# Performance work log

Measured on AMD Instinct MI355X. Metric: run time of the kernel, lower is better.

## Reference

```python
import jax, jax.numpy as jnp
import numpy as np

B, S, D, J, NI = 8192, 20, 300, 512, 1000
VG = 2048 + 5 * 6  # vis_dim + 5*6 = guide feature dim


def setup_inputs() -> dict:
    key = jax.random.key(0)
    ks = jax.random.split(key, 11)
    context = jax.random.normal(ks[0], (B, S, D), jnp.float32)
    embedded = jax.random.normal(ks[1], (B, S, D), jnp.float32)
    input_labels = jax.random.randint(ks[2], (B, S), 0, 10000, dtype=jnp.int64)
    # guarantee at least one valid token per row (avoid divide-by-zero renorm)
    input_labels = input_labels.at[:, 0].set(jnp.maximum(input_labels[:, 0], 1))
    guide_input = jax.random.normal(ks[3], (NI, VG), jnp.float32)
    sent_to_image_ann = jax.random.randint(ks[4], (2 * B,), 0, NI, dtype=jnp.int64)
    # parameters (PyTorch Linear: y = x @ W.T + b)
    W_sent = jax.random.normal(ks[5], (J, D), jnp.float32) * 0.02
    b_sent = jnp.zeros((J,), jnp.float32)
    W_emb = jax.random.normal(ks[6], (J, VG), jnp.float32) * 0.02
    b_emb = jnp.zeros((J,), jnp.float32)
    w_fc = jax.random.normal(ks[7], (J,), jnp.float32) * 0.02
    b_fc = jnp.zeros((), jnp.float32)
    return {"context": context, "embedded": embedded, "input_labels": input_labels,
            "guide_input": guide_input, "sent_to_image_ann": sent_to_image_ann,
            "W_sent": W_sent, "b_sent": b_sent, "W_emb": W_emb, "b_emb": b_emb,
            "w_fc": w_fc, "b_fc": b_fc}


def reference(context, embedded, input_labels, guide_input, sent_to_image_ann,
              W_sent, b_sent, W_emb, b_emb, w_fc, b_fc):
    # prefix-valid mask: loop in original breaks at first zero label
    nonzero = (input_labels != 0).astype(jnp.float32)          # (B,S)
    valid = jnp.cumprod(nonzero, axis=1)                        # (B,S)
    # per-sentence guide feature: guide_input[sent_to_image_ann[2*i]]
    fea = guide_input[sent_to_image_ann[::2]]                   # (B,VG)
    # fc_embed(guidance): guidance rows are fea (valid prefix) or 0 (else),
    # so the linear output is fea@W_emb.T+b_emb or just b_emb.
    fea_emb = fea @ W_emb.T + b_emb                             # (B,J)
    guid_emb = valid[:, :, None] * fea_emb[:, None, :] + (1.0 - valid)[:, :, None] * b_emb
    cxt_emb = jnp.einsum('bsd,jd->bsj', context, W_sent) + b_sent
    H = jnp.tanh(cxt_emb + guid_emb)                            # (B,S,J)
    scores = jnp.einsum('bsj,j->bs', H, w_fc) + b_fc            # (B,S)
    attn = jax.nn.softmax(scores, axis=1)
    attn = attn * nonzero
    attn = attn / jnp.sum(attn, axis=1, keepdims=True)
    weighted_cxt = jnp.einsum('bs,bsd->bd', attn, embedded)     # (B,D)
    return weighted_cxt
```

## Files before the change

### kernel.cpp

```cpp
#include <hip/hip_runtime.h>
#include <hip/hip_bf16.h>

#define BB 8192
#define SS 20
#define DD 300
#define JJ 512
#define NII 1000
#define VGG 2078
#define KP 328
#define RBY 656
#define BTILE 41984
#define BP1 72

typedef __attribute__((ext_vector_type(8))) short short8v;
typedef __attribute__((ext_vector_type(4))) float float4v;

__device__ __forceinline__ float tanh_fast(float x) {
    float t = __expf(2.f * x);
    return 1.f - 2.f * __builtin_amdgcn_rcpf(t + 1.f);
}

__device__ __forceinline__ unsigned short bf16u(float x) {
    __hip_bfloat16 h = __float2bfloat16(x);
    return *(unsigned short*)&h;
}

__device__ __forceinline__ void gload16(const void* g, void* l) {
    __builtin_amdgcn_global_load_lds(
        (const __attribute__((address_space(1))) unsigned int*)g,
        (__attribute__((address_space(3))) unsigned int*)l, 16, 0, 0);
}

__global__ __launch_bounds__(256) void kc_pad_bf16(const float* __restrict__ src,
                                                   __hip_bfloat16* __restrict__ dst,
                                                   int rows, int scols, int dcols) {
    int idx = blockIdx.x * 256 + threadIdx.x;
    if (idx >= rows * dcols) return;
    int r = idx / dcols, c = idx % dcols;
    float v = (c < scols) ? src[(long)r * scols + c] : 0.f;
    dst[idx] = __float2bfloat16(v);
}

__global__ __launch_bounds__(256) void k0_valid(const int* __restrict__ labels,
                                                float* __restrict__ valid,
                                                float* __restrict__ nonzero) {
    int b = blockIdx.x * blockDim.x + threadIdx.x;
    if (b >= BB) return;
    float v = 1.f;
    for (int s = 0; s < SS; ++s) {
        float nz = (labels[b * SS + s] != 0) ? 1.f : 0.f;
        v *= nz;
        nonzero[b * SS + s] = nz;
        valid[b * SS + s] = v;
    }
}

__global__ __launch_bounds__(256) void k1_femb_mfma(
    const __hip_bfloat16* __restrict__ Gb,
    const __hip_bfloat16* __restrict__ Web,
    const float* __restrict__ b_emb,
    __hip_bfloat16* __restrict__ femb) {
    __shared__ __hip_bfloat16 Al[64 * BP1];
    __shared__ __hip_bfloat16 Bl[64 * BP1];
    const int t = threadIdx.x;
    const int m0 = blockIdx.x * 64;
    const int n0 = blockIdx.y * 64;
    const int lane = t & 63;
    const int w = t >> 6;
    const int wm = w >> 1, wn = w & 1;
    const int li = lane & 15, lq = lane >> 4;

    float4v acc[2][2] = {};

    for (int kt = 0; kt < 33; ++kt) {
        for (int c = t; c < 512; c += 256) {
            int rr = c >> 3, off = (c & 7) * 8;
            int gr = m0 + rr; if (gr > NII - 1) gr = NII - 1;
            *(uint4*)&Al[rr * BP1 + off] =
                *(const uint4*)(Gb + (long)gr * 2112 + kt * 64 + off);
            *(uint4*)&Bl[rr * BP1 + off] =
                *(const uint4*)(Web + (long)(n0 + rr) * 2112 + kt * 64 + off);
        }
        __syncthreads();
#pragma unroll
        for (int ks = 0; ks < 2; ++ks) {
            short8v a[2], b[2];
#pragma unroll
            for (int mt = 0; mt < 2; ++mt)
                a[mt] = *(const short8v*)&Al[(wm * 32 + mt * 16 + li) * BP1 + ks * 32 + lq * 8];
#pragma unroll
            for (int nt = 0; nt < 2; ++nt)
                b[nt] = *(const short8v*)&Bl[(wn * 32 + nt * 16 + li) * BP1 + ks * 32 + lq * 8];
#pragma unroll
            for (int mt = 0; mt < 2; ++mt)
#pragma unroll
                for (int nt = 0; nt < 2; ++nt)
                    acc[mt][nt] = __builtin_amdgcn_mfma_f32_16x16x32_bf16(
                        a[mt], b[nt], acc[mt][nt], 0, 0, 0);
        }
        __syncthreads();
    }
#pragma unroll
    for (int nt = 0; nt < 2; ++nt) {
        int col = n0 + wn * 32 + nt * 16 + li;
        float be = b_emb[col];
#pragma unroll
        for (int mt = 0; mt < 2; ++mt)
#pragma unroll
            for (int reg = 0; reg < 4; ++reg) {
                int row = wm * 32 + mt * 16 + lq * 4 + reg;
                femb[(long)(m0 + row) * JJ + col] = __float2bfloat16(acc[mt][nt][reg] + be);
            }
    }
}

__global__ __launch_bounds__(256) void k2_scores_mfma(
    const float* __restrict__ context,
    const __hip_bfloat16* __restrict__ Wsb,
    const float* __restrict__ b_sent,
    const float* __restrict__ w_fc,
    const float* __restrict__ b_fc,
    const __hip_bfloat16* __restrict__ femb,
    const int* __restrict__ ann,
    const float* __restrict__ b_emb,
    const float* __restrict__ valid,
    float* __restrict__ scores) {
    __shared__ __align__(16) char smem[48128];
    char* buf  = smem;
    char* fl   = smem + 41984;
    float* red = (float*)(smem + 47104);

    const int t = threadIdx.x;
    const int m0 = blockIdx.x * 64;
    const int b_lo = m0 / SS;
    const int lane = t & 63;
    const int w = t >> 6;
    const int wm = w >> 1, wn = w & 1;
    const int li = lane & 15, lq = lane >> 4;

    for (int idx = t; idx < 64 * 82; idx += 256) {
        int r = idx / 82, q = idx - r * 82;
        ushort4 pk;
        if (q < 75) {
            float4 v = *(const float4*)(context + (long)(m0 + r) * DD + q * 4);
            pk.x = bf16u(v.x); pk.y = bf16u(v.y); pk.z = bf16u(v.z); pk.w = bf16u(v.w);
        } else { pk.x = pk.y = pk.z = pk.w = 0; }
        *(ushort4*)(buf + r * RBY + q * 8) = pk;
    }
    if (t < 320) {
        int i = t >> 6, ch = t & 63;
        int b = b_lo + i; if (b > BB - 1) b = BB - 1;
        int grow = ann[2 * b];
        *(uint4*)(fl + i * 1024 + ch * 16) =
            *(const uint4*)(femb + (long)grow * JJ + ch * 8);
    }
    int brel0_0 = 0, brel0_1 = 0, selbits = 0, vbits = 0;
#pragma unroll
    for (int mt = 0; mt < 2; ++mt) {
        int base = m0 + wm * 32 + mt * 16 + lq * 4;
        int br0 = base / SS - b_lo;
        if (mt == 0) brel0_0 = br0; else brel0_1 = br0;
#pragma unroll
        for (int reg = 0; reg < 4; ++reg) {
            int m = base + reg;
            int slot = mt * 4 + reg;
            if (m / SS - b_lo != br0) selbits |= (1 << slot);
            if (valid[m] != 0.f)      vbits  |= (1 << slot);
        }
    }
    __syncthreads();

    short8v areg[2][10];
#pragma unroll
    for (int mt = 0; mt < 2; ++mt) {
        int r = wm * 32 + mt * 16 + li;
#pragma unroll
        for (int kt = 0; kt < 10; ++kt)
            areg[mt][kt] = *(const short8v*)(buf + r * RBY + kt * 64 + lq * 16);
    }
    __syncthreads();

    float sp[8] = {0.f, 0.f, 0.f, 0.f, 0.f, 0.f, 0.f, 0.f};
    const int rbB0 = (wn * 32 + li) * RBY;
    const int rbB1 = (wn * 32 + 16 + li) * RBY;

    for (int jt = 0; jt < 8; ++jt) {
        const char* gB = (const char*)Wsb + (long)jt * BTILE;
        const int wbase = w * 656;
#pragma unroll
        for (int i = 0; i < 10; ++i)
            gload16(gB + (long)(wbase + i * 64 + lane) * 16,
                    buf + (wbase + i * 64) * 16);
        if (lane < 16)
            gload16(gB + (long)(wbase + 640 + lane) * 16,
                    buf + (wbase + 640) * 16);
        __syncthreads();

        float4v acc[2][2] = {};
#pragma unroll
        for (int kt = 0; kt < 10; ++kt) {
            short8v b0 = *(const short8v*)(buf + rbB0 + kt * 64 + lq * 16);
            short8v b1 = *(const short8v*)(buf + rbB1 + kt * 64 + lq * 16);
            acc[0][0] = __builtin_amdgcn_mfma_f32_16x16x32_bf16(areg[0][kt], b0, acc[0][0], 0, 0, 0);
            acc[0][1] = __builtin_amdgcn_mfma_f32_16x16x32_bf16(areg[0][kt], b1, acc[0][1], 0, 0, 0);
            acc[1][0] = __builtin_amdgcn_mfma_f32_16x16x32_bf16(areg[1][kt], b0, acc[1][0], 0, 0, 0);
            acc[1][1] = __builtin_amdgcn_mfma_f32_16x16x32_bf16(areg[1][kt], b1, acc[1][1], 0, 0, 0);
        }

#pragma unroll
        for (int nt = 0; nt < 2; ++nt) {
            int col = jt * 64 + wn * 32 + nt * 16 + li;
            float bs = b_sent[col], wf = w_fc[col], be = b_emb[col];
#pragma unroll
            for (int mt = 0; mt < 2; ++mt) {
                int br = (mt == 0) ? brel0_0 : brel0_1;
                int br1 = (br < 4) ? br + 1 : 4;
                float f0 = __bfloat162float(*(const __hip_bfloat16*)(fl + br  * 1024 + col * 2));
                float f1 = __bfloat162float(*(const __hip_bfloat16*)(fl + br1 * 1024 + col * 2));
#pragma unroll
                for (int reg = 0; reg < 4; ++reg) {
                    int slot = mt * 4 + reg;
                    float fv = ((selbits >> slot) & 1) ? f1 : f0;
                    float g  = ((vbits  >> slot) & 1) ? fv : be;
                    sp[slot] += tanh_fast(acc[mt][nt][reg] + bs + g) * wf;
                }
            }
        }
        __syncthreads();
    }

#pragma unroll
    for (int slot = 0; slot < 8; ++slot) {
        float v = sp[slot];
        v += __shfl_xor(v, 1); v += __shfl_xor(v, 2);
        v += __shfl_xor(v, 4); v += __shfl_xor(v, 8);
        sp[slot] = v;
    }
    if (li == 0) {
#pragma unroll
        for (int mt = 0; mt < 2; ++mt)
#pragma unroll
            for (int reg = 0; reg < 4; ++reg)
                red[wn * 64 + wm * 32 + mt * 16 + lq * 4 + reg] = sp[mt * 4 + reg];
    }
    __syncthreads();
    if (t < 64) scores[m0 + t] = red[t] + red[64 + t] + b_fc[0];
}

__global__ __launch_bounds__(256) void k3_out(const float* __restrict__ scores,
                                              const float* __restrict__ nonzero,
                                              const float* __restrict__ embedded,
                                              float* __restrict__ out) {
    __shared__ float wgt[3][SS];
    const int b0 = blockIdx.x * 3;
    const int t = threadIdx.x;
    if (t < 3) {
        int b = b0 + t;
        if (b < BB) {
            float sc[SS], nz[SS];
            float mx = -1e30f;
            for (int s = 0; s < SS; ++s) {
                sc[s] = scores[b * SS + s];
                nz[s] = nonzero[b * SS + s];
                mx = fmaxf(mx, sc[s]);
            }
            float den = 0.f, e[SS];
            for (int s = 0; s < SS; ++s) { e[s] = nz[s] * __expf(sc[s] - mx); den += e[s]; }
            float inv = 1.f / den;
            for (int s = 0; s < SS; ++s) wgt[t][s] = e[s] * inv;
        }
    }
    __syncthreads();
    if (t < 225) {
        int r = t / 75, q = t - r * 75;
        int b = b0 + r;
        if (b < BB) {
            float4 a; a.x = a.y = a.z = a.w = 0.f;
#pragma unroll
            for (int s = 0; s < SS; ++s) {
                float4 e = *(const float4*)(embedded + ((long)b * SS + s) * DD + q * 4);
                float ww = wgt[r][s];
                a.x += ww * e.x; a.y += ww * e.y; a.z += ww * e.z; a.w += ww * e.w;
            }
            *(float4*)(out + (long)b * DD + q * 4) = a;
        }
    }
}

extern "C" void kernel_launch(void* const* d_in, const int* in_sizes, int n_in,
                              void* d_out, int out_size, void* d_ws, size_t ws_size,
                              hipStream_t stream) {
    const float* context  = (const float*)d_in[0];
    const float* embedded = (const float*)d_in[1];
    const int*   labels   = (const int*)d_in[2];
    const float* guide    = (const float*)d_in[3];
    const int*   ann      = (const int*)d_in[4];
    const float* W_sent   = (const float*)d_in[5];
    const float* b_sent   = (const float*)d_in[6];
    const float* W_emb    = (const float*)d_in[7];
    const float* b_emb    = (const float*)d_in[8];
    const float* w_fc     = (const float*)d_in[9];
    const float* b_fc     = (const float*)d_in[10];
    float* out = (float*)d_out;

    char* w = (char*)d_ws;
    __hip_bfloat16* femb = (__hip_bfloat16*)(w);
    float* valid         = (float*)(w + 1048576);
    float* nonzero       = (float*)(w + 1703936);
    float* scores        = (float*)(w + 2359296);
    __hip_bfloat16* Wsb  = (__hip_bfloat16*)(w + 3014656);
    __hip_bfloat16* Web  = (__hip_bfloat16*)(w + 3350528);
    __hip_bfloat16* Gb   = (__hip_bfloat16*)(w + 5513216);

    hipLaunchKernelGGL(kc_pad_bf16, dim3((JJ * KP + 255) / 256), dim3(256), 0, stream,
                       W_sent, Wsb, JJ, DD, KP);
    hipLaunchKernelGGL(kc_pad_bf16, dim3((JJ * 2112 + 255) / 256), dim3(256), 0, stream,
                       W_emb, Web, JJ, VGG, 2112);
    hipLaunchKernelGGL(kc_pad_bf16, dim3((NII * 2112 + 255) / 256), dim3(256), 0, stream,
                       guide, Gb, NII, VGG, 2112);
    hipLaunchKernelGGL(k0_valid, dim3(BB / 256), dim3(256), 0, stream,
                       labels, valid, nonzero);
    hipLaunchKernelGGL(k1_femb_mfma, dim3(16, JJ / 64), dim3(256), 0, stream,
                       Gb, Web, b_emb, femb);
    hipLaunchKernelGGL(k2_scores_mfma, dim3((BB * SS) / 64), dim3(256), 0, stream,
                       context, Wsb, b_sent, w_fc, b_fc, femb, ann, b_emb, valid, scores);
    hipLaunchKernelGGL(k3_out, dim3((BB + 2) / 3), dim3(256), 0, stream,
                       scores, nonzero, embedded, out);
}
```

Before: 250.0 us.

## Fold biases into GEMM K-padding, rewrite tanh sum algebraically, load B directly

The scores kernel now places b_sent and b_emb into the padded K columns of the bf16 W_sent matrix. The context tile gets matching 1 and (1-valid) entries, so the MFMA produces the bias terms itself. The tanh-weighted sum becomes sum(w_fc) - 2*sum(w_fc/(1+e^{2x})), using a precomputed sum(w_fc) from a new tiny kernel, which removes per-element ops. The per-tile B operand is read straight from global memory into registers instead of staged through LDS with barriers, and the guide feature rows are kept as fp32 in LDS. This trades LDS sharing and barrier sync for repeated global/L2 reads per wave, and adds bf16 rounding of the biases.

```diff
diff --git a/kernel.cpp b/kernel.cpp
--- a/kernel.cpp
+++ b/kernel.cpp
@@ -10,25 +10,18 @@
 #define KP 328
 #define RBY 656
 #define BTILE 41984
+#define FLP 516
 #define BP1 72
 
 typedef __attribute__((ext_vector_type(8))) short short8v;
 typedef __attribute__((ext_vector_type(4))) float float4v;
-
-__device__ __forceinline__ float tanh_fast(float x) {
-    float t = __expf(2.f * x);
-    return 1.f - 2.f * __builtin_amdgcn_rcpf(t + 1.f);
-}
 
 __device__ __forceinline__ unsigned short bf16u(float x) {
     __hip_bfloat16 h = __float2bfloat16(x);
     return *(unsigned short*)&h;
 }
-
-__device__ __forceinline__ void gload16(const void* g, void* l) {
-    __builtin_amdgcn_global_load_lds(
-        (const __attribute__((address_space(1))) unsigned int*)g,
-        (__attribute__((address_space(3))) unsigned int*)l, 16, 0, 0);
+__device__ __forceinline__ float bfraw2f(unsigned short u) {
+    return __uint_as_float((unsigned)u << 16);
 }
 
 __global__ __launch_bounds__(256) void kc_pad_bf16(const float* __restrict__ src,
@@ -39,6 +32,36 @@
     int r = idx / dcols, c = idx % dcols;
     float v = (c < scols) ? src[(long)r * scols + c] : 0.f;
     dst[idx] = __float2bfloat16(v);
+}
+
+__global__ __launch_bounds__(256) void kc_prep_wsb(const float* __restrict__ W_sent,
+                                                   const float* __restrict__ b_sent,
+                                                   const float* __restrict__ b_emb,
+                                                   __hip_bfloat16* __restrict__ dst) {
+    int idx = blockIdx.x * 256 + threadIdx.x;
+    if (idx >= JJ * KP) return;
+    int j = idx / KP, c = idx % KP;
+    float v = (c < DD) ? W_sent[(long)j * DD + c]
+            : (c == DD) ? b_sent[j]
+            : (c == DD + 1) ? b_emb[j] : 0.f;
+    dst[idx] = __float2bfloat16(v);
+}
+
+__global__ __launch_bounds__(512) void kS_sumwf(const float* __restrict__ w_fc,
+                                                float* __restrict__ out) {
+    __shared__ float part[8];
+    int t = threadIdx.x;
+    float v = w_fc[t];
+    v += __shfl_xor(v, 1);  v += __shfl_xor(v, 2);  v += __shfl_xor(v, 4);
+    v += __shfl_xor(v, 8);  v += __shfl_xor(v, 16); v += __shfl_xor(v, 32);
+    if ((t & 63) == 0) part[t >> 6] = v;
+    __syncthreads();
+    if (t == 0) {
+        float s = 0.f;
+#pragma unroll
+        for (int i = 0; i < 8; ++i) s += part[i];
+        out[0] = s;
+    }
 }
 
 __global__ __launch_bounds__(256) void k0_valid(const int* __restrict__ labels,
@@ -117,18 +140,16 @@
 __global__ __launch_bounds__(256) void k2_scores_mfma(
     const float* __restrict__ context,
     const __hip_bfloat16* __restrict__ Wsb,
-    const float* __restrict__ b_sent,
     const float* __restrict__ w_fc,
     const float* __restrict__ b_fc,
+    const float* __restrict__ sumwf,
     const __hip_bfloat16* __restrict__ femb,
     const int* __restrict__ ann,
-    const float* __restrict__ b_emb,
     const float* __restrict__ valid,
     float* __restrict__ scores) {
-    __shared__ __align__(16) char smem[48128];
-    char* buf  = smem;
-    char* fl   = smem + 41984;
-    float* red = (float*)(smem + 47104);
+    __shared__ __align__(16) char smem[41984 + 5 * FLP * 4];
+    char* buf = smem;
+    float* fl = (float*)(smem + 41984);
 
     const int t = threadIdx.x;
     const int m0 = blockIdx.x * 64;
@@ -144,6 +165,8 @@
         if (q < 75) {
             float4 v = *(const float4*)(context + (long)(m0 + r) * DD + q * 4);
             pk.x = bf16u(v.x); pk.y = bf16u(v.y); pk.z = bf16u(v.z); pk.w = bf16u(v.w);
+        } else if (q == 75) {
+            pk.x = bf16u(1.f); pk.y = bf16u(1.f - valid[m0 + r]); pk.z = 0; pk.w = 0;
         } else { pk.x = pk.y = pk.z = pk.w = 0; }
         *(ushort4*)(buf + r * RBY + q * 8) = pk;
     }
@@ -151,21 +174,27 @@
         int i = t >> 6, ch = t & 63;
         int b = b_lo + i; if (b > BB - 1) b = BB - 1;
         int grow = ann[2 * b];
-        *(uint4*)(fl + i * 1024 + ch * 16) =
-            *(const uint4*)(femb + (long)grow * JJ + ch * 8);
-    }
-    int brel0_0 = 0, brel0_1 = 0, selbits = 0, vbits = 0;
+        short8v rv = *(const short8v*)(femb + (long)grow * JJ + ch * 8);
+        float4 lo, hi;
+        lo.x = bfraw2f((unsigned short)rv[0]); lo.y = bfraw2f((unsigned short)rv[1]);
+        lo.z = bfraw2f((unsigned short)rv[2]); lo.w = bfraw2f((unsigned short)rv[3]);
+        hi.x = bfraw2f((unsigned short)rv[4]); hi.y = bfraw2f((unsigned short)rv[5]);
+        hi.z = bfraw2f((unsigned short)rv[6]); hi.w = bfraw2f((unsigned short)rv[7]);
+        *(float4*)(fl + i * FLP + ch * 8)     = lo;
+        *(float4*)(fl + i * FLP + ch * 8 + 4) = hi;
+    }
+    float vm[8]; int selb = 0; int br_[2];
 #pragma unroll
     for (int mt = 0; mt < 2; ++mt) {
         int base = m0 + wm * 32 + mt * 16 + lq * 4;
         int br0 = base / SS - b_lo;
-        if (mt == 0) brel0_0 = br0; else brel0_1 = br0;
+        br_[mt] = br0;
 #pragma unroll
         for (int reg = 0; reg < 4; ++reg) {
             int m = base + reg;
             int slot = mt * 4 + reg;
-            if (m / SS - b_lo != br0) selbits |= (1 << slot);
-            if (valid[m] != 0.f)      vbits  |= (1 << slot);
+            if (m / SS - b_lo != br0) selb |= (1 << slot);
+            vm[slot] = valid[m];
         }
     }
     __syncthreads();
@@ -178,73 +207,80 @@
         for (int kt = 0; kt < 10; ++kt)
             areg[mt][kt] = *(const short8v*)(buf + r * RBY + kt * 64 + lq * 16);
     }
-    __syncthreads();
-
-    float sp[8] = {0.f, 0.f, 0.f, 0.f, 0.f, 0.f, 0.f, 0.f};
-    const int rbB0 = (wn * 32 + li) * RBY;
-    const int rbB1 = (wn * 32 + 16 + li) * RBY;
+
+    float sp2[8] = {0.f, 0.f, 0.f, 0.f, 0.f, 0.f, 0.f, 0.f};
+    const char* pB = (const char*)Wsb + (wn * 32 + li) * RBY + lq * 16;
 
     for (int jt = 0; jt < 8; ++jt) {
-        const char* gB = (const char*)Wsb + (long)jt * BTILE;
-        const int wbase = w * 656;
-#pragma unroll
-        for (int i = 0; i < 10; ++i)
-            gload16(gB + (long)(wbase + i * 64 + lane) * 16,
-                    buf + (wbase + i * 64) * 16);
-        if (lane < 16)
-            gload16(gB + (long)(wbase + 640 + lane) * 16,
-                    buf + (wbase + 640) * 16);
-        __syncthreads();
-
+        const char* pj = pB + (long)jt * BTILE;
         float4v acc[2][2] = {};
-#pragma unroll
-        for (int kt = 0; kt < 10; ++kt) {
-            short8v b0 = *(const short8v*)(buf + rbB0 + kt * 64 + lq * 16);
-            short8v b1 = *(const short8v*)(buf + rbB1 + kt * 64 + lq * 16);
-            acc[0][0] = __builtin_amdgcn_mfma_f32_16x16x32_bf16(areg[0][kt], b0, acc[0][0], 0, 0, 0);
-            acc[0][1] = __builtin_amdgcn_mfma_f32_16x16x32_bf16(areg[0][kt], b1, acc[0][1], 0, 0, 0);
-            acc[1][0] = __builtin_amdgcn_mfma_f32_16x16x32_bf16(areg[1][kt], b0, acc[1][0], 0, 0, 0);
-            acc[1][1] = __builtin_amdgcn_mfma_f32_16x16x32_bf16(areg[1][kt], b1, acc[1][1], 0, 0, 0);
-        }
-
+        short8v bf0[5], bf1[5];
+#pragma unroll
+        for (int kt = 0; kt < 5; ++kt) {
+            bf0[kt] = *(const short8v*)(pj + kt * 64);
+            bf1[kt] = *(const short8v*)(pj + 16 * RBY + kt * 64);
+        }
+#pragma unroll
+        for (int kt = 0; kt < 5; ++kt) {
+            acc[0][0] = __builtin_amdgcn_mfma_f32_16x16x32_bf16(areg[0][kt], bf0[kt], acc[0][0], 0, 0, 0);
+            acc[0][1] = __builtin_amdgcn_mfma_f32_16x16x32_bf16(areg[0][kt], bf1[kt], acc[0][1], 0, 0, 0);
+            acc[1][0] = __builtin_amdgcn_mfma_f32_16x16x32_bf16(areg[1][kt], bf0[kt], acc[1][0], 0, 0, 0);
+            acc[1][1] = __builtin_amdgcn_mfma_f32_16x16x32_bf16(areg[1][kt], bf1[kt], acc[1][1], 0, 0, 0);
+        }
+#pragma unroll
+        for (int kt = 0; kt < 5; ++kt) {
+            bf0[kt] = *(const short8v*)(pj + 320 + kt * 64);
+            bf1[kt] = *(const short8v*)(pj + 16 * RBY + 320 + kt * 64);
+        }
+#pragma unroll
+        for (int kt = 0; kt < 5; ++kt) {
+            acc[0][0] = __builtin_amdgcn_mfma_f32_16x16x32_bf16(areg[0][5 + kt], bf0[kt], acc[0][0], 0, 0, 0);
+            acc[0][1] = __builtin_amdgcn_mfma_f32_16x16x32_bf16(areg[0][5 + kt], bf1[kt], acc[0][1], 0, 0, 0);
+            acc[1][0] = __builtin_amdgcn_mfma_f32_16x16x32_bf16(areg[1][5 + kt], bf0[kt], acc[1][0], 0, 0, 0);
+            acc[1][1] = __builtin_amdgcn_mfma_f32_16x16x32_bf16(areg[1][5 + kt], bf1[kt], acc[1][1], 0, 0, 0);
+        }
 #pragma unroll
         for (int nt = 0; nt < 2; ++nt) {
             int col = jt * 64 + wn * 32 + nt * 16 + li;
-            float bs = b_sent[col], wf = w_fc[col], be = b_emb[col];
+            float wf = w_fc[col];
 #pragma unroll
             for (int mt = 0; mt < 2; ++mt) {
-                int br = (mt == 0) ? brel0_0 : brel0_1;
+                int br = br_[mt];
                 int br1 = (br < 4) ? br + 1 : 4;
-                float f0 = __bfloat162float(*(const __hip_bfloat16*)(fl + br  * 1024 + col * 2));
-                float f1 = __bfloat162float(*(const __hip_bfloat16*)(fl + br1 * 1024 + col * 2));
+                float f0 = fl[br * FLP + col];
+                float f1 = fl[br1 * FLP + col];
 #pragma unroll
                 for (int reg = 0; reg < 4; ++reg) {
                     int slot = mt * 4 + reg;
-                    float fv = ((selbits >> slot) & 1) ? f1 : f0;
-                    float g  = ((vbits  >> slot) & 1) ? fv : be;
-                    sp[slot] += tanh_fast(acc[mt][nt][reg] + bs + g) * wf;
+                    float fv = ((selb >> slot) & 1) ? f1 : f0;
+                    float x = acc[mt][nt][reg] + vm[slot] * fv;
+                    float e = __expf(2.f * x);
+                    float r = __builtin_amdgcn_rcpf(e + 1.f);
+                    sp2[slot] += wf * r;
                 }
             }
         }
-        __syncthreads();
     }
 
 #pragma unroll
     for (int slot = 0; slot < 8; ++slot) {
-        float v = sp[slot];
+        float v = sp2[slot];
         v += __shfl_xor(v, 1); v += __shfl_xor(v, 2);
         v += __shfl_xor(v, 4); v += __shfl_xor(v, 8);
-        sp[slot] = v;
-    }
+        sp2[slot] = v;
+    }
+    __syncthreads();
+    float* red = (float*)smem;
     if (li == 0) {
 #pragma unroll
         for (int mt = 0; mt < 2; ++mt)
 #pragma unroll
             for (int reg = 0; reg < 4; ++reg)
-                red[wn * 64 + wm * 32 + mt * 16 + lq * 4 + reg] = sp[mt * 4 + reg];
-    }
-    __syncthreads();
-    if (t < 64) scores[m0 + t] = red[t] + red[64 + t] + b_fc[0];
+                red[wn * 64 + wm * 32 + mt * 16 + lq * 4 + reg] = sp2[mt * 4 + reg];
+    }
+    __syncthreads();
+    if (t < 64)
+        scores[m0 + t] = b_fc[0] + sumwf[0] - 2.f * (red[t] + red[64 + t]);
 }
 
 __global__ __launch_bounds__(256) void k3_out(const float* __restrict__ scores,
@@ -311,19 +347,21 @@
     __hip_bfloat16* Wsb  = (__hip_bfloat16*)(w + 3014656);
     __hip_bfloat16* Web  = (__hip_bfloat16*)(w + 3350528);
     __hip_bfloat16* Gb   = (__hip_bfloat16*)(w + 5513216);
-
-    hipLaunchKernelGGL(kc_pad_bf16, dim3((JJ * KP + 255) / 256), dim3(256), 0, stream,
-                       W_sent, Wsb, JJ, DD, KP);
+    float* sums          = (float*)(w + 9737216);
+
+    hipLaunchKernelGGL(kc_prep_wsb, dim3((JJ * KP + 255) / 256), dim3(256), 0, stream,
+                       W_sent, b_sent, b_emb, Wsb);
     hipLaunchKernelGGL(kc_pad_bf16, dim3((JJ * 2112 + 255) / 256), dim3(256), 0, stream,
                        W_emb, Web, JJ, VGG, 2112);
     hipLaunchKernelGGL(kc_pad_bf16, dim3((NII * 2112 + 255) / 256), dim3(256), 0, stream,
                        guide, Gb, NII, VGG, 2112);
+    hipLaunchKernelGGL(kS_sumwf, dim3(1), dim3(512), 0, stream, w_fc, sums);
     hipLaunchKernelGGL(k0_valid, dim3(BB / 256), dim3(256), 0, stream,
                        labels, valid, nonzero);
     hipLaunchKernelGGL(k1_femb_mfma, dim3(16, JJ / 64), dim3(256), 0, stream,
                        Gb, Web, b_emb, femb);
     hipLaunchKernelGGL(k2_scores_mfma, dim3((BB * SS) / 64), dim3(256), 0, stream,
-                       context, Wsb, b_sent, w_fc, b_fc, femb, ann, b_emb, valid, scores);
+                       context, Wsb, w_fc, b_fc, sums, femb, ann, valid, scores);
     hipLaunchKernelGGL(k3_out, dim3((BB + 2) / 3), dim3(256), 0, stream,
                        scores, nonzero, embedded, out);
 }
```

Measured after the change: 282.6 us. +13.0%, slower.
